# Performance work log

Hardware: AMD Instinct MI355X
Metric: run time of the kernel (lower is better)

The kernel has to match this reference:

```python
import jax, jax.numpy as jnp
import numpy as np

NEG_SLOPE = 0.2  # PyG GATConv default negative_slope


def _gat_conv(x, edge_index, W, att_src, att_dst, bias, heads, out_ch, concat):
    """PyG-style GATConv with add_self_loops=False, shared src/dst lin.
    x: [N, F_in], edge_index: [2, E] (row 0 = src j, row 1 = dst i).
    W: [F_in, heads*out_ch]; att_src/att_dst: [heads, out_ch]; bias: [heads*out_ch] or [out_ch].
    """
    N = x.shape[0]
    src, dst = edge_index[0], edge_index[1]
    h = (x @ W).reshape(N, heads, out_ch)                      # [N, H, C]
    a_src = jnp.einsum('nhc,hc->nh', h, att_src)               # [N, H]
    a_dst = jnp.einsum('nhc,hc->nh', h, att_dst)               # [N, H]
    e = a_src[src] + a_dst[dst]                                # [E, H]
    e = jnp.where(e > 0, e, NEG_SLOPE * e)                     # leaky_relu
    # segment softmax over edges sharing the same destination
    m = jax.ops.segment_max(e, dst, num_segments=N)            # [N, H]
    e = jnp.exp(e - m[dst])                                    # [E, H]
    s = jax.ops.segment_sum(e, dst, num_segments=N)            # [N, H]
    alpha = e / (s[dst] + 1e-16)                               # [E, H]
    msg = h[src] * alpha[:, :, None]                           # [E, H, C]
    out = jax.ops.segment_sum(msg, dst, num_segments=N)        # [N, H, C]
    if concat:
        out = out.reshape(N, heads * out_ch)
    else:
        out = out.mean(axis=1)
    return out + bias


def setup_inputs() -> dict:
    key = jax.random.key(0)
    ks = jax.random.split(key, 12)
    N, E = 100000, 1600000
    dinp, dhid, dout, heads = 128, 32, 128, 4
    x = jax.random.normal(ks[0], (N, dinp), dtype=jnp.float32)
    a = jax.random.randint(ks[1], (2, E), 0, N, dtype=jnp.int64)
    s1 = 1.0 / np.sqrt(dinp)
    s2 = 1.0 / np.sqrt(dhid * heads)
    return {
        'x': x,
        'a': a,
        'W1': jax.random.normal(ks[2], (dinp, heads * dhid), dtype=jnp.float32) * s1,
        'att_src1': jax.random.normal(ks[3], (heads, dhid), dtype=jnp.float32) * s1,
        'att_dst1': jax.random.normal(ks[4], (heads, dhid), dtype=jnp.float32) * s1,
        'b1': jnp.zeros((heads * dhid,), dtype=jnp.float32),
        'W2': jax.random.normal(ks[5], (heads * dhid, dout), dtype=jnp.float32) * s2,
        'att_src2': jax.random.normal(ks[6], (1, dout), dtype=jnp.float32) * s2,
        'att_dst2': jax.random.normal(ks[7], (1, dout), dtype=jnp.float32) * s2,
        'b2': jnp.zeros((dout,), dtype=jnp.float32),
    }


def reference(x, a, W1, att_src1, att_dst1, b1, W2, att_src2, att_dst2, b2):
    heads, dhid, dout = 4, 32, 128
    h = _gat_conv(x, a, W1, att_src1, att_dst1, b1, heads, dhid, concat=True)
    h = jax.nn.elu(h)
    out = _gat_conv(h, a, W2, att_src2, att_dst2, b2, 1, dout, concat=False)
    return jax.nn.elu(out)
```

## Files before the change

### kernel.cpp

```cpp
#include <hip/hip_runtime.h>
#include <hip/hip_fp16.h>
#include <math.h>


typedef _Float16 f16x8 __attribute__((ext_vector_type(8)));
typedef float    f32x4 __attribute__((ext_vector_type(4)));


__global__ __launch_bounds__(256) void k_hist(const int* __restrict__ dst,
                                              int* __restrict__ bcnt, int E, int NBUCK) {
    __shared__ int lh[1024];
    int t = threadIdx.x;
    for (int i = t; i < NBUCK; i += 256) lh[i] = 0;
    __syncthreads();
    for (int e = blockIdx.x * 256 + t; e < E; e += gridDim.x * 256)
        atomicAdd(&lh[dst[e] >> 7], 1);
    __syncthreads();
    for (int i = t; i < NBUCK; i += 256) {
        int c = lh[i];
        if (c) atomicAdd(&bcnt[i], c);
    }
}

__global__ void k_bscan(const int* __restrict__ bcnt, int* __restrict__ bbase,
                        int* __restrict__ bcur, int* __restrict__ off,
                        int NBUCK, int N, int E) {
    __shared__ int sd[1024];
    int t = threadIdx.x;
    int v = (t < NBUCK) ? bcnt[t] : 0;
    sd[t] = v; __syncthreads();
    for (int ofs = 1; ofs < 1024; ofs <<= 1) {
        int w = (t >= ofs) ? sd[t - ofs] : 0;
        __syncthreads();
        sd[t] += w;
        __syncthreads();
    }
    if (t < NBUCK) { int ex = sd[t] - v; bbase[t] = ex; bcur[t] = ex; }
    if (t == 0) { bbase[NBUCK] = E; off[N] = E; }
}

__global__ __launch_bounds__(256) void k_binscatter(
    const int* __restrict__ src, const int* __restrict__ dst,
    int* __restrict__ bcur, int* __restrict__ tmp, int E, int NBUCK) {
    __shared__ int lh[1024], lbase[1024];
    int t = threadIdx.x;
    for (int i = t; i < NBUCK; i += 256) lh[i] = 0;
    __syncthreads();
    int tbeg = blockIdx.x * 8192;
    int tend = tbeg + 8192; if (tend > E) tend = E;
    for (int e = tbeg + t; e < tend; e += 256) atomicAdd(&lh[dst[e] >> 7], 1);
    __syncthreads();
    for (int i = t; i < NBUCK; i += 256) {
        int c = lh[i];
        lbase[i] = c ? atomicAdd(&bcur[i], c) : 0;
        lh[i] = 0;
    }
    __syncthreads();
    for (int e = tbeg + t; e < tend; e += 256) {
        int d = dst[e];
        int b = d >> 7;
        int r = atomicAdd(&lh[b], 1);
        tmp[lbase[b] + r] = (src[e] << 7) | (d & 127);
    }
}

__global__ __launch_bounds__(256) void k_bsort(
    const int* __restrict__ tmp, const int* __restrict__ bbase,
    int* __restrict__ off, int* __restrict__ esrc, int N) {
    __shared__ int h[128], hs[128], cur[128];
    int b = blockIdx.x, t = threadIdx.x;
    int base = bbase[b];
    int cnt  = bbase[b + 1] - base;
    int node0 = b << 7;
    if (t < 128) h[t] = 0;
    __syncthreads();
    for (int i = t; i < cnt; i += 256) atomicAdd(&h[tmp[base + i] & 127], 1);
    __syncthreads();
    if (t < 128) hs[t] = h[t];
    __syncthreads();
    for (int ofs = 1; ofs < 128; ofs <<= 1) {
        int w = (t < 128 && t >= ofs) ? hs[t - ofs] : 0;
        __syncthreads();
        if (t < 128) hs[t] += w;
        __syncthreads();
    }
    if (t < 128) {
        int ex = hs[t] - h[t];
        if (node0 + t < N) off[node0 + t] = base + ex;
        cur[t] = base + ex;
    }
    __syncthreads();
    for (int i = t; i < cnt; i += 256) {
        int p = tmp[base + i];
        int pos = atomicAdd(&cur[p & 127], 1);
        esrc[pos] = p >> 7;
    }
}


template <int H, typename TI>
__global__ __launch_bounds__(256, 2) void k_gemm_mfma(
    const TI* __restrict__ X, const float* __restrict__ Wg,
    const float* __restrict__ att_s, const float* __restrict__ att_d,
    __half* __restrict__ Y, float* __restrict__ as_, float* __restrict__ ad_, int N)
{
    __shared__ _Float16 Wh[128 * 128];
    __shared__ _Float16 Xh[64][136];
    const int t = threadIdx.x;
    const int lane = t & 63;
    const int wv = t >> 6;
    const int m = lane & 15;
    const int q = lane >> 4;

    for (int i = t; i < 128 * 128 / 4; i += 256) {
        float4 w4 = ((const float4*)Wg)[i];
        _Float16* d = &Wh[i * 4];
        d[0] = (_Float16)w4.x; d[1] = (_Float16)w4.y;
        d[2] = (_Float16)w4.z; d[3] = (_Float16)w4.w;
    }
    __syncthreads();

    f16x8 bfr[8][4];
#pragma unroll
    for (int nt = 0; nt < 8; nt++) {
#pragma unroll
        for (int ks = 0; ks < 4; ks++) {
            f16x8 b;
#pragma unroll
            for (int j = 0; j < 8; j++)
                b[j] = Wh[(ks * 32 + q * 8 + j) * 128 + nt * 16 + m];
            bfr[nt][ks] = b;
        }
    }
    float atts_v[8], attd_v[8];
#pragma unroll
    for (int nt = 0; nt < 8; nt++) {
        atts_v[nt] = att_s[nt * 16 + m];
        attd_v[nt] = att_d[nt * 16 + m];
    }

    for (int base = blockIdx.x * 64; base < N; base += gridDim.x * 64) {
        for (int i = t; i < 1024; i += 256) {
            int r = i >> 4, c8 = i & 15;
            int gr = base + r;
            _Float16* d = &Xh[r][c8 * 8];
            if (gr < N) {
                if constexpr (sizeof(TI) == 4) {
                    const float4* s = (const float4*)((const float*)X + (size_t)gr * 128 + c8 * 8);
                    float4 x0 = s[0], x1 = s[1];
                    d[0] = (_Float16)x0.x; d[1] = (_Float16)x0.y;
                    d[2] = (_Float16)x0.z; d[3] = (_Float16)x0.w;
                    d[4] = (_Float16)x1.x; d[5] = (_Float16)x1.y;
                    d[6] = (_Float16)x1.z; d[7] = (_Float16)x1.w;
                } else {
                    *(uint4*)d = *(const uint4*)((const __half*)X + (size_t)gr * 128 + c8 * 8);
                }
            } else {
                uint4 z; z.x = 0; z.y = 0; z.z = 0; z.w = 0;
                *(uint4*)d = z;
            }
        }
        __syncthreads();

        const int rowb = base + wv * 16;
        f32x4 acc[8];
#pragma unroll
        for (int nt = 0; nt < 8; nt++) { acc[nt][0] = 0.f; acc[nt][1] = 0.f; acc[nt][2] = 0.f; acc[nt][3] = 0.f; }
#pragma unroll
        for (int ks = 0; ks < 4; ks++) {
            f16x8 af = *(const f16x8*)&Xh[wv * 16 + m][ks * 32 + q * 8];
#pragma unroll
            for (int nt = 0; nt < 8; nt++)
                acc[nt] = __builtin_amdgcn_mfma_f32_16x16x32_f16(af, bfr[nt][ks], acc[nt], 0, 0, 0);
        }

#pragma unroll
        for (int nt = 0; nt < 8; nt++) {
#pragma unroll
            for (int i = 0; i < 4; i++) {
                int r = rowb + q * 4 + i;
                if (r < N) Y[(size_t)r * 128 + nt * 16 + m] = __float2half(acc[nt][i]);
            }
        }

        if (H == 4) {
            float ph[4][4], pdv[4][4];
#pragma unroll
            for (int h = 0; h < 4; h++)
#pragma unroll
                for (int i = 0; i < 4; i++) {
                    ph[h][i]  = acc[2 * h][i] * atts_v[2 * h] + acc[2 * h + 1][i] * atts_v[2 * h + 1];
                    pdv[h][i] = acc[2 * h][i] * attd_v[2 * h] + acc[2 * h + 1][i] * attd_v[2 * h + 1];
                }
#pragma unroll
            for (int lvl = 0; lvl < 4; lvl++) {
                const int msk = 1 << lvl;
#pragma unroll
                for (int h = 0; h < 4; h++)
#pragma unroll
                    for (int i = 0; i < 4; i++) {
                        ph[h][i]  += __shfl_xor(ph[h][i], msk, 64);
                        pdv[h][i] += __shfl_xor(pdv[h][i], msk, 64);
                    }
            }
            if (m == 0) {
#pragma unroll
                for (int i = 0; i < 4; i++) {
                    int r = rowb + q * 4 + i;
                    if (r < N) {
#pragma unroll
                        for (int h = 0; h < 4; h++) {
                            as_[(size_t)r * 4 + h] = ph[h][i];
                            ad_[(size_t)r * 4 + h] = pdv[h][i];
                        }
                    }
                }
            }
        } else {
            float ps[4], pdv[4];
#pragma unroll
            for (int i = 0; i < 4; i++) {
                float s = 0.f, dsum = 0.f;
#pragma unroll
                for (int nt = 0; nt < 8; nt++) {
                    s    += acc[nt][i] * atts_v[nt];
                    dsum += acc[nt][i] * attd_v[nt];
                }
                ps[i] = s; pdv[i] = dsum;
            }
#pragma unroll
            for (int lvl = 0; lvl < 4; lvl++) {
                const int msk = 1 << lvl;
#pragma unroll
                for (int i = 0; i < 4; i++) {
                    ps[i]  += __shfl_xor(ps[i], msk, 64);
                    pdv[i] += __shfl_xor(pdv[i], msk, 64);
                }
            }
            if (m == 0) {
#pragma unroll
                for (int i = 0; i < 4; i++) {
                    int r = rowb + q * 4 + i;
                    if (r < N) { as_[r] = ps[i]; ad_[r] = pdv[i]; }
                }
            }
        }
        __syncthreads();
    }
}


template <int H, typename TO>
__global__ __launch_bounds__(256) void k_agg(
    const __half* __restrict__ feat,
    const float* __restrict__ asrc,
    const float* __restrict__ adst,
    const int*   __restrict__ off,
    const int*   __restrict__ esrc,
    const float* __restrict__ bias,
    TO*          __restrict__ out,
    int N)
{
    __shared__ __attribute__((aligned(16))) int   sj[4][64];
    __shared__ __attribute__((aligned(16))) float sp[4][64 * H];

    int wave = threadIdx.x >> 6;
    int lane = threadIdx.x & 63;
    int node = (blockIdx.x * 256 + threadIdx.x) >> 6;
    if (node >= N) return;
    int beg = off[node], end = off[node + 1];

    float adst_i[H];
#pragma unroll
    for (int h = 0; h < H; h++) adst_i[h] = adst[(size_t)node * H + h];

    const int g    = lane >> 4;
    const int sub  = lane & 15;
    const int head = (H == 4) ? (sub >> 2) : 0;
    const __half* fb = feat + sub * 8;

    float o[8];
#pragma unroll
    for (int k = 0; k < 8; k++) o[k] = 0.f;
    float ssum = 0.f;

    for (int cbeg = beg; cbeg < end; cbeg += 64) {
        int cnt = end - cbeg; if (cnt > 64) cnt = 64;
        if (lane < cnt) {
            int j = esrc[cbeg + lane];
            sj[wave][lane] = j;
            if (H == 4) {
                float4 av = *(const float4*)(asrc + (size_t)j * 4);
                float e;
                e = av.x + adst_i[0]; e = e > 0.f ? e : 0.2f * e; sp[wave][0 * 64 + lane] = __expf(e);
                e = av.y + adst_i[1]; e = e > 0.f ? e : 0.2f * e; sp[wave][1 * 64 + lane] = __expf(e);
                e = av.z + adst_i[2]; e = e > 0.f ? e : 0.2f * e; sp[wave][2 * 64 + lane] = __expf(e);
                e = av.w + adst_i[3]; e = e > 0.f ? e : 0.2f * e; sp[wave][3 * 64 + lane] = __expf(e);
            } else {
                float e = asrc[j] + adst_i[0];
                e = e > 0.f ? e : 0.2f * e;
                sp[wave][lane] = __expf(e);
            }
        }
        asm volatile("s_waitcnt lgkmcnt(0)" ::: "memory");

        for (int b0 = 0; b0 < cnt; b0 += 16) {
            float aa[4]; uint4 hv[4];
#pragma unroll
            for (int u = 0; u < 4; u++) {
                int e  = b0 + 4 * u + g;
                bool ok = e < cnt;
                int ec = ok ? e : 0;
                int j  = sj[wave][ec];
                aa[u]  = ok ? sp[wave][head * 64 + ec] : 0.f;
                hv[u]  = *(const uint4*)(fb + (size_t)j * 128);
            }
#pragma unroll
            for (int u = 0; u < 4; u++) {
                const __half* hp = (const __half*)&hv[u];
                ssum += aa[u];
#pragma unroll
                for (int k = 0; k < 8; k++)
                    o[k] = fmaf(aa[u], __half2float(hp[k]), o[k]);
            }
        }
    }

#pragma unroll
    for (int k = 0; k < 8; k++) {
        o[k] += __shfl_xor(o[k], 16, 64);
        o[k] += __shfl_xor(o[k], 32, 64);
    }
    ssum += __shfl_xor(ssum, 16, 64);
    ssum += __shfl_xor(ssum, 32, 64);

    if (g == 0) {
        float inv = 1.f / (ssum + 1e-16f);
        float r[8];
#pragma unroll
        for (int k = 0; k < 8; k++) {
            r[k] = o[k] * inv + bias[sub * 8 + k];
            r[k] = r[k] > 0.f ? r[k] : expm1f(r[k]);
        }
        if constexpr (sizeof(TO) == 2) {
            __half2 hh[4];
#pragma unroll
            for (int p = 0; p < 4; p++) hh[p] = __floats2half2_rn(r[2 * p], r[2 * p + 1]);
            *(uint4*)((__half*)out + (size_t)node * 128 + sub * 8) = *(const uint4*)hh;
        } else {
            float4 v0 = make_float4(r[0], r[1], r[2], r[3]);
            float4 v1 = make_float4(r[4], r[5], r[6], r[7]);
            *(float4*)((float*)out + (size_t)node * 128 + sub * 8)     = v0;
            *(float4*)((float*)out + (size_t)node * 128 + sub * 8 + 4) = v1;
        }
    }
}


extern "C" void kernel_launch(void* const* d_in, const int* in_sizes, int n_in,
                              void* d_out, int out_size, void* d_ws, size_t ws_size,
                              hipStream_t stream)
{
    const float* x    = (const float*)d_in[0];
    const int*   a    = (const int*)  d_in[1];
    const float* W1   = (const float*)d_in[2];
    const float* as1w = (const float*)d_in[3];
    const float* ad1w = (const float*)d_in[4];
    const float* b1   = (const float*)d_in[5];
    const float* W2   = (const float*)d_in[6];
    const float* as2w = (const float*)d_in[7];
    const float* ad2w = (const float*)d_in[8];
    const float* b2   = (const float*)d_in[9];

    const int N = in_sizes[0] / 128;
    const int E = in_sizes[1] / 2;
    const int* srcA = a;
    const int* dstA = a + E;
    const int NBUCK = (N + 127) >> 7;

    char* ws = (char*)d_ws;
    size_t o = 0;
    auto alloc = [&](size_t bytes) -> void* {
        void* p = ws + o;
        o += (bytes + 255) & ~(size_t)255;
        return p;
    };
    __half* hbuf  = (__half*)alloc((size_t)N * 128 * 2);
    __half* hact  = (__half*)alloc((size_t)N * 128 * 2);
    float*  as1   = (float*) alloc((size_t)N * 4 * 4);
    float*  ad1   = (float*) alloc((size_t)N * 4 * 4);
    float*  as2   = (float*) alloc((size_t)N * 4);
    float*  ad2   = (float*) alloc((size_t)N * 4);
    int*    off   = (int*)   alloc((size_t)(N + 1) * 4);
    int*    esrc  = (int*)   alloc((size_t)E * 4);
    int*    tmp   = (int*)   alloc((size_t)E * 4);
    int*    bcnt  = (int*)   alloc(1024 * 4);
    int*    bbase = (int*)   alloc(1025 * 4);
    int*    bcur  = (int*)   alloc(1024 * 4);

    hipMemsetAsync(bcnt, 0, (size_t)NBUCK * 4, stream);
    k_hist<<<256, 256, 0, stream>>>(dstA, bcnt, E, NBUCK);
    k_bscan<<<1, 1024, 0, stream>>>(bcnt, bbase, bcur, off, NBUCK, N, E);
    k_binscatter<<<(E + 8191) / 8192, 256, 0, stream>>>(srcA, dstA, bcur, tmp, E, NBUCK);
    k_bsort<<<NBUCK, 256, 0, stream>>>(tmp, bbase, off, esrc, N);

    k_gemm_mfma<4, float><<<512, 256, 0, stream>>>(x, W1, as1w, ad1w, hbuf, as1, ad1, N);
    k_agg<4, __half><<<(N + 3) / 4, 256, 0, stream>>>(hbuf, as1, ad1, off, esrc, b1, hact, N);

    k_gemm_mfma<1, __half><<<512, 256, 0, stream>>>(hact, W2, as2w, ad2w, hbuf, as2, ad2, N);
    k_agg<1, float><<<(N + 3) / 4, 256, 0, stream>>>(hbuf, as2, ad2, off, esrc, b2, (float*)d_out, N);
}
```

Measured before the change: 405.6 us.

## Prefetch next feature gather batch and broadcast source indices via shuffles

Source indices now stay in registers and are broadcast with wave shuffles instead of being staged through shared memory. The first batch of half-precision feature rows is gathered before the attention exponentials are computed, and each later batch is loaded while the FMAs for the current one run. The aim is to hide gather latency in the aggregation kernel. It costs more registers for the double-buffered loads, which may lower occupancy.

```diff
diff --git a/kernel.cpp b/kernel.cpp
--- a/kernel.cpp
+++ b/kernel.cpp
@@ -261,7 +261,6 @@
     TO*          __restrict__ out,
     int N)
 {
-    __shared__ __attribute__((aligned(16))) int   sj[4][64];
     __shared__ __attribute__((aligned(16))) float sp[4][64 * H];
 
     int wave = threadIdx.x >> 6;
@@ -286,9 +285,18 @@
 
     for (int cbeg = beg; cbeg < end; cbeg += 64) {
         int cnt = end - cbeg; if (cnt > 64) cnt = 64;
+
+        int j = 0;
+        if (lane < cnt) j = esrc[cbeg + lane];
+
+        uint4 hv[4];
+#pragma unroll
+        for (int u = 0; u < 4; u++) {
+            int jj = __shfl(j, 4 * u + g, 64);
+            hv[u] = *(const uint4*)(fb + (size_t)jj * 128);
+        }
+
         if (lane < cnt) {
-            int j = esrc[cbeg + lane];
-            sj[wave][lane] = j;
             if (H == 4) {
                 float4 av = *(const float4*)(asrc + (size_t)j * 4);
                 float e;
@@ -304,16 +312,22 @@
         }
         asm volatile("s_waitcnt lgkmcnt(0)" ::: "memory");
 
-        for (int b0 = 0; b0 < cnt; b0 += 16) {
-            float aa[4]; uint4 hv[4];
+        const int nb = (cnt + 15) >> 4;
+        for (int b = 0; b < nb; b++) {
+            const int b0 = b << 4;
+            float aa[4];
 #pragma unroll
             for (int u = 0; u < 4; u++) {
-                int e  = b0 + 4 * u + g;
-                bool ok = e < cnt;
-                int ec = ok ? e : 0;
-                int j  = sj[wave][ec];
-                aa[u]  = ok ? sp[wave][head * 64 + ec] : 0.f;
-                hv[u]  = *(const uint4*)(fb + (size_t)j * 128);
+                int e = b0 + 4 * u + g;
+                aa[u] = (e < cnt) ? sp[wave][head * 64 + e] : 0.f;
+            }
+            uint4 nv[4];
+            if (b + 1 < nb) {
+#pragma unroll
+                for (int u = 0; u < 4; u++) {
+                    int jj = __shfl(j, b0 + 16 + 4 * u + g, 64);
+                    nv[u] = *(const uint4*)(fb + (size_t)jj * 128);
+                }
             }
 #pragma unroll
             for (int u = 0; u < 4; u++) {
@@ -322,6 +336,10 @@
 #pragma unroll
                 for (int k = 0; k < 8; k++)
                     o[k] = fmaf(aa[u], __half2float(hp[k]), o[k]);
+            }
+            if (b + 1 < nb) {
+#pragma unroll
+                for (int u = 0; u < 4; u++) hv[u] = nv[u];
             }
         }
     }
```

Result: slower. 506.5 us (+24.9%).

## Fuse layer-1 GEMM with destination histogram into one heterogeneous launch

Applied to the files above, without the earlier changes.

Merges the edge-destination histogram kernel and the first-layer MFMA GEMM into a single 768-block launch. Two of every three blocks run the GEMM body and the third runs the histogram body. The intent is to overlap the memory-bound histogram with the compute-heavy GEMM and drop one launch. In exchange the histogram blocks now reserve the GEMM's large shared-memory footprint, which may lower their occupancy, and the GEMM is now ordered before the sort stages.

```diff
diff --git a/kernel.cpp b/kernel.cpp
--- a/kernel.cpp
+++ b/kernel.cpp
@@ -7,13 +7,14 @@
 typedef float    f32x4 __attribute__((ext_vector_type(4)));
 
 
-__global__ __launch_bounds__(256) void k_hist(const int* __restrict__ dst,
-                                              int* __restrict__ bcnt, int E, int NBUCK) {
+__device__ __forceinline__ void hist_body(const int* __restrict__ dst,
+                                          int* __restrict__ bcnt, int E, int NBUCK,
+                                          int hb, int hnb) {
     __shared__ int lh[1024];
     int t = threadIdx.x;
     for (int i = t; i < NBUCK; i += 256) lh[i] = 0;
     __syncthreads();
-    for (int e = blockIdx.x * 256 + t; e < E; e += gridDim.x * 256)
+    for (int e = hb * 256 + t; e < E; e += hnb * 256)
         atomicAdd(&lh[dst[e] >> 7], 1);
     __syncthreads();
     for (int i = t; i < NBUCK; i += 256) {
@@ -99,10 +100,11 @@
 
 
 template <int H, typename TI>
-__global__ __launch_bounds__(256, 2) void k_gemm_mfma(
+__device__ __forceinline__ void gemm_mfma_body(
     const TI* __restrict__ X, const float* __restrict__ Wg,
     const float* __restrict__ att_s, const float* __restrict__ att_d,
-    __half* __restrict__ Y, float* __restrict__ as_, float* __restrict__ ad_, int N)
+    __half* __restrict__ Y, float* __restrict__ as_, float* __restrict__ ad_,
+    int N, int gb, int gnb)
 {
     __shared__ _Float16 Wh[128 * 128];
     __shared__ _Float16 Xh[64][136];
@@ -139,7 +141,7 @@
         attd_v[nt] = att_d[nt * 16 + m];
     }
 
-    for (int base = blockIdx.x * 64; base < N; base += gridDim.x * 64) {
+    for (int base = gb * 64; base < N; base += gnb * 64) {
         for (int i = t; i < 1024; i += 256) {
             int r = i >> 4, c8 = i & 15;
             int gr = base + r;
@@ -246,6 +248,31 @@
             }
         }
         __syncthreads();
+    }
+}
+
+template <int H, typename TI>
+__global__ __launch_bounds__(256, 2) void k_gemm_mfma(
+    const TI* __restrict__ X, const float* __restrict__ Wg,
+    const float* __restrict__ att_s, const float* __restrict__ att_d,
+    __half* __restrict__ Y, float* __restrict__ as_, float* __restrict__ ad_, int N)
+{
+    gemm_mfma_body<H, TI>(X, Wg, att_s, att_d, Y, as_, ad_, N, blockIdx.x, gridDim.x);
+}
+
+__global__ __launch_bounds__(256, 2) void k_g1_hist(
+    const float* __restrict__ X, const float* __restrict__ Wg,
+    const float* __restrict__ att_s, const float* __restrict__ att_d,
+    __half* __restrict__ Y, float* __restrict__ as_, float* __restrict__ ad_, int N,
+    const int* __restrict__ dst, int* __restrict__ bcnt, int E, int NBUCK)
+{
+    const int bid = blockIdx.x;
+    const int r = bid % 3;
+    if (r < 2) {
+        gemm_mfma_body<4, float>(X, Wg, att_s, att_d, Y, as_, ad_, N,
+                                 (bid / 3) * 2 + r, 512);
+    } else {
+        hist_body(dst, bcnt, E, NBUCK, bid / 3, 256);
     }
 }
 
@@ -399,12 +426,14 @@
     int*    bcur  = (int*)   alloc(1024 * 4);
 
     hipMemsetAsync(bcnt, 0, (size_t)NBUCK * 4, stream);
-    k_hist<<<256, 256, 0, stream>>>(dstA, bcnt, E, NBUCK);
+
+    k_g1_hist<<<768, 256, 0, stream>>>(x, W1, as1w, ad1w, hbuf, as1, ad1, N,
+                                       dstA, bcnt, E, NBUCK);
+
     k_bscan<<<1, 1024, 0, stream>>>(bcnt, bbase, bcur, off, NBUCK, N, E);
     k_binscatter<<<(E + 8191) / 8192, 256, 0, stream>>>(srcA, dstA, bcur, tmp, E, NBUCK);
     k_bsort<<<NBUCK, 256, 0, stream>>>(tmp, bbase, off, esrc, N);
 
-    k_gemm_mfma<4, float><<<512, 256, 0, stream>>>(x, W1, as1w, ad1w, hbuf, as1, ad1, N);
     k_agg<4, __half><<<(N + 3) / 4, 256, 0, stream>>>(hbuf, as1, ad1, off, esrc, b1, hact, N);
 
     k_gemm_mfma<1, __half><<<512, 256, 0, stream>>>(hact, W2, as2w, ad2w, hbuf, as2, ad2, N);
```

Result: no change. 410.6 us (+1.2%).
